# Kernel tuning notes

Hardware: AMD Instinct MI355X
Metric: run time of the kernel (lower is better)

Reference implementation:

```python
import jax, jax.numpy as jnp
import numpy as np

PI2 = 2.0 * np.pi
ZITTER = 1e-4
TEMP = 0.1          # tempering0
LIKERR_BOUND = (0.1, 1.0)
GUMBEL_EPS = 1e-20


def setup_inputs() -> dict:
    key = jax.random.key(0)
    ks = jax.random.split(key, 12)
    nb, nd, ndim, nch = 8, 768, 1, 3
    nmix, h, ns = 5, 10, 10
    def xavier(k, shape):
        fan_in, fan_out = shape[1], shape[0]
        lim = np.sqrt(6.0 / (fan_in + fan_out))
        return jax.random.uniform(k, shape, jnp.float32, -lim, lim)
    return {
        "xc": jax.random.normal(ks[0], (nb, nd, ndim, nch), jnp.float32),
        "yc": jax.random.normal(ks[1], (nb, nd, nch), jnp.float32),
        "mu": jax.random.uniform(ks[2], (nmix, ndim), jnp.float32),
        "inv_std": jax.random.uniform(ks[3], (nmix, ndim), jnp.float32),
        "likerr": jax.random.uniform(ks[4], (nch,), jnp.float32),
        "unif": jax.random.uniform(ks[5], (nb, ns, nch, nmix), jnp.float32),
        "W1": xavier(ks[6], (h, nmix + 1)), "b1": jnp.zeros((h,), jnp.float32),
        "W2": xavier(ks[7], (h, h * nch)), "b2": jnp.zeros((h,), jnp.float32),
        "W3": xavier(ks[8], (h, h)), "b3": jnp.zeros((h,), jnp.float32),
        "W4": xavier(ks[9], (h, h)), "b4": jnp.zeros((h,), jnp.float32),
        "W5": xavier(ks[10], (nmix * nch, h)), "b5": jnp.zeros((nmix * nch,), jnp.float32),
    }


def _sm_kernel_mix(xc, mu, inv_std):
    """Spectral-mixture kernel per mixture: (nb,nmix,nd,nd,nch)."""
    exp_x = xc[:, None] * inv_std[None, :, None, :, None]   # (nb,nmix,nd,ndim,nch)
    cos_x = xc[:, None] * mu[None, :, None, :, None]
    e2 = jnp.sum(exp_x ** 2, axis=-2)                        # (nb,nmix,nd,nch)
    cross = jnp.einsum('bmadk,bmcdk->bmack', exp_x, exp_x)   # (nb,nmix,nd,nd,nch)
    exp_term = e2[:, :, :, None, :] + e2[:, :, None, :, :] - 2.0 * cross
    c1 = jnp.sum(cos_x, axis=-2)                             # (nb,nmix,nd,nch)
    cos_term = c1[:, :, :, None, :] - c1[:, :, None, :, :]
    return jnp.exp(-0.5 * PI2 ** 2 * exp_term) * jnp.cos(PI2 * cos_term)


def reference(xc, yc, mu, inv_std, likerr, unif,
              W1, b1, W2, b2, W3, b3, W4, b4, W5, b5):
    nb, nd, ndim, nch = xc.shape
    nmix = mu.shape[0]
    outs = _sm_kernel_mix(xc, mu, inv_std)                   # (nb,nmix,nd,nd,nch)

    # --- trans-invariant weight net (logits=None kernel path + zitter eye) ---
    # feature[b,i,c,m] = sum_j (K + zitter*I)[b,m,i,j,c] * yc[b,j,c]
    feature = jnp.einsum('bmijc,bjc->bicm', outs, yc) + ZITTER * yc[:, :, :, None]
    tif = jnp.concatenate([feature, yc[..., None]], axis=-1) # (nb,nd,nch,nmix+1)
    hh = jax.nn.relu(tif @ W1.T + b1)                        # (nb,nd,nch,h)
    hh = hh.mean(axis=1).reshape(nb, -1)                     # (nb,nch*h)
    hh = jax.nn.relu(hh @ W2.T + b2)
    hh = jax.nn.relu(hh @ W3.T + b3)
    hh = jax.nn.relu(hh @ W4.T + b4)
    loglogits = (hh @ W5.T + b5).reshape(nb, nch, nmix)      # (nb,nch,nmix)

    # --- Gumbel-softmax mixture sampling ---
    g = -jnp.log(-jnp.log(unif + GUMBEL_EPS))                # (nb,ns,nch,nmix)
    y = jax.nn.softmax((g + loglogits[:, None]) / TEMP, axis=-1)
    logits_s = y.mean(axis=1)                                # (nb,nch,nmix)

    # --- weighted mixture reduction + noise diagonal ---
    w = jnp.transpose(logits_s, (0, 2, 1))[:, :, None, None, :]  # (nb,nmix,1,1,nch)
    weighted = jnp.sum(outs * w, axis=1)                     # (nb,nd,nd,nch)
    likerr_c = jnp.clip(likerr, LIKERR_BOUND[0], LIKERR_BOUND[1])
    eye = jnp.eye(nd, dtype=xc.dtype)
    weighted = weighted + (ZITTER + likerr_c ** 2)[None, None, None, :] * eye[None, :, :, None]
    return weighted
```

## Files before the change

kernel.cpp:

```cpp
#include <hip/hip_runtime.h>
#include <hip/hip_bf16.h>

#define NB 8
#define ND 768
#define NCH 3
#define NMIX 5
#define NH 10
#define NS 10

#define PI2F 6.283185307179586f
#define HALF_PI2SQ 19.739208802178716f
#define ZITTERF 1e-4f

__device__ __forceinline__ float cos2pi(float t) {
    return __builtin_amdgcn_cosf(__builtin_amdgcn_fractf(t));
}

__global__ void __launch_bounds__(256) feature_kernel(
        const float* __restrict__ xc, const float* __restrict__ yc,
        const float* __restrict__ mu, const float* __restrict__ istd,
        float* __restrict__ tif) {
    const int wid  = (blockIdx.x << 2) + (threadIdx.x >> 6);
    const int lane = threadIdx.x & 63;
    const int b   = wid / (ND * NCH);
    const int rem = wid % (ND * NCH);
    const int i = rem / NCH;
    const int c = rem % NCH;

    float cmu[NMIX], cexp[NMIX];
#pragma unroll
    for (int m = 0; m < NMIX; ++m) {
        const float is = istd[m];
        cmu[m]  = mu[m];
        cexp[m] = -HALF_PI2SQ * is * is;
    }

    const float xi = xc[(b * ND + i) * NCH + c];
    float acc[NMIX] = {0.f, 0.f, 0.f, 0.f, 0.f};

    for (int j = lane; j < ND; j += 64) {
        const float xj = xc[(b * ND + j) * NCH + c];
        const float yj = yc[(b * ND + j) * NCH + c];
        const float dx  = xi - xj;
        const float dx2 = dx * dx;
#pragma unroll
        for (int m = 0; m < NMIX; ++m) {
            const float e  = __expf(cexp[m] * dx2);
            const float co = cos2pi(cmu[m] * dx);
            acc[m] += e * co * yj;
        }
    }

#pragma unroll
    for (int m = 0; m < NMIX; ++m)
        for (int off = 32; off; off >>= 1)
            acc[m] += __shfl_down(acc[m], off);

    if (lane == 0) {
        const float yi = yc[(b * ND + i) * NCH + c];
        float* tp = tif + ((b * ND + i) * NCH + c) * (NMIX + 1);
#pragma unroll
        for (int m = 0; m < NMIX; ++m) tp[m] = acc[m] + ZITTERF * yi;
        tp[NMIX] = yi;
    }
}

__global__ void __launch_bounds__(256) mlp_gumbel_kernel(
        const float* __restrict__ tif,
        const float* __restrict__ W1, const float* __restrict__ b1,
        const float* __restrict__ W2, const float* __restrict__ b2,
        const float* __restrict__ W3, const float* __restrict__ b3,
        const float* __restrict__ W4, const float* __restrict__ b4,
        const float* __restrict__ W5, const float* __restrict__ b5,
        const float* __restrict__ unif,
        float* __restrict__ wout) {
    const int b   = blockIdx.x;
    const int tid = threadIdx.x;

    __shared__ float sW1[NH * 6], sb1[NH];
    __shared__ float red[4][NCH * NH];
    __shared__ float hvec[NCH * NH], h2[NH], h3[NH], h4[NH], ll[NCH * NMIX], wacc[NCH * NMIX];

    if (tid < NH * 6) sW1[tid] = W1[tid];
    if (tid < NH)     sb1[tid] = b1[tid];
    if (tid < NCH * NMIX) wacc[tid] = 0.f;
    __syncthreads();

    float part[NCH * NH];
#pragma unroll
    for (int t = 0; t < NCH * NH; ++t) part[t] = 0.f;

    for (int ii = tid; ii < ND; ii += 256) {
        for (int c = 0; c < NCH; ++c) {
            const float* tp = tif + ((b * ND + ii) * NCH + c) * (NMIX + 1);
            float f[6];
#pragma unroll
            for (int m = 0; m < 6; ++m) f[m] = tp[m];
#pragma unroll
            for (int k = 0; k < NH; ++k) {
                float a = sb1[k];
#pragma unroll
                for (int m = 0; m < 6; ++m) a += f[m] * sW1[k * 6 + m];
                part[c * NH + k] += fmaxf(a, 0.f);
            }
        }
    }

#pragma unroll
    for (int t = 0; t < NCH * NH; ++t)
        for (int off = 32; off; off >>= 1)
            part[t] += __shfl_down(part[t], off);

    const int lane = tid & 63, wv = tid >> 6;
    if (lane == 0)
        for (int t = 0; t < NCH * NH; ++t) red[wv][t] = part[t];
    __syncthreads();

    if (tid < NCH * NH)
        hvec[tid] = (red[0][tid] + red[1][tid] + red[2][tid] + red[3][tid]) * (1.f / (float)ND);
    __syncthreads();

    if (tid < NH) {
        float a = b2[tid];
        for (int j = 0; j < NCH * NH; ++j) a += W2[tid * (NCH * NH) + j] * hvec[j];
        h2[tid] = fmaxf(a, 0.f);
    }
    __syncthreads();
    if (tid < NH) {
        float a = b3[tid];
        for (int j = 0; j < NH; ++j) a += W3[tid * NH + j] * h2[j];
        h3[tid] = fmaxf(a, 0.f);
    }
    __syncthreads();
    if (tid < NH) {
        float a = b4[tid];
        for (int j = 0; j < NH; ++j) a += W4[tid * NH + j] * h3[j];
        h4[tid] = fmaxf(a, 0.f);
    }
    __syncthreads();
    if (tid < NCH * NMIX) {
        float a = b5[tid];
        for (int j = 0; j < NH; ++j) a += W5[tid * NH + j] * h4[j];
        ll[tid] = a;
    }
    __syncthreads();

    if (tid < NS * NCH) {
        const int s = tid / NCH, c = tid % NCH;
        float z[NMIX], zmax = -1e30f;
#pragma unroll
        for (int m = 0; m < NMIX; ++m) {
            const float u = unif[((b * NS + s) * NCH + c) * NMIX + m];
            const float g = -__logf(-__logf(u + 1e-20f));
            z[m] = (g + ll[c * NMIX + m]) * 10.0f;
            zmax = fmaxf(zmax, z[m]);
        }
        float e[NMIX], se = 0.f;
#pragma unroll
        for (int m = 0; m < NMIX; ++m) { e[m] = __expf(z[m] - zmax); se += e[m]; }
        const float inv = 0.1f / se;
#pragma unroll
        for (int m = 0; m < NMIX; ++m)
            atomicAdd(&wacc[c * NMIX + m], e[m] * inv);
    }
    __syncthreads();
    if (tid < NCH * NMIX) wout[b * (NCH * NMIX) + tid] = wacc[tid];
}

__global__ void __launch_bounds__(256) weighted_kernel(
        const float* __restrict__ xc, const float* __restrict__ wmix,
        const float* __restrict__ mu, const float* __restrict__ istd,
        const float* __restrict__ likerr,
        float* __restrict__ out) {
    const int b   = blockIdx.x / ((ND * ND) / 256);
    const int rem = blockIdx.x % ((ND * ND) / 256);
    const int i   = rem / (ND / 256);
    const int j   = (rem % (ND / 256)) * 256 + threadIdx.x;
    const int tid = threadIdx.x;

    __shared__ float sw[NCH * NMIX], smu[NMIX], sce[NMIX], sdiag[NCH], sxi[NCH];
    if (tid < NCH * NMIX) sw[tid] = wmix[b * (NCH * NMIX) + tid];
    if (tid < NMIX) {
        smu[tid] = mu[tid];
        const float is = istd[tid];
        sce[tid] = -HALF_PI2SQ * is * is;
    }
    if (tid < NCH) {
        const float lk = fminf(fmaxf(likerr[tid], 0.1f), 1.0f);
        sdiag[tid] = ZITTERF + lk * lk;
        sxi[tid]   = xc[(b * ND + i) * NCH + tid];
    }
    __syncthreads();

    float xj[NCH];
#pragma unroll
    for (int c = 0; c < NCH; ++c) xj[c] = xc[(b * ND + j) * NCH + c];

    float res[NCH];
#pragma unroll
    for (int c = 0; c < NCH; ++c) {
        const float dx  = sxi[c] - xj[c];
        const float dx2 = dx * dx;
        float a = 0.f;
#pragma unroll
        for (int m = 0; m < NMIX; ++m)
            a += sw[c * NMIX + m] * __expf(sce[m] * dx2) * cos2pi(smu[m] * dx);
        if (i == j) a += sdiag[c];
        res[c] = a;
    }

    float* op = out + (size_t)((b * ND + i) * ND + j) * NCH;
    op[0] = res[0];
    op[1] = res[1];
    op[2] = res[2];
}

extern "C" void kernel_launch(void* const* d_in, const int* in_sizes, int n_in,
                              void* d_out, int out_size, void* d_ws, size_t ws_size,
                              hipStream_t stream) {
    const float* xc     = (const float*)d_in[0];
    const float* yc     = (const float*)d_in[1];
    const float* mu     = (const float*)d_in[2];
    const float* istd   = (const float*)d_in[3];
    const float* likerr = (const float*)d_in[4];
    const float* unif   = (const float*)d_in[5];
    const float* W1 = (const float*)d_in[6];  const float* b1 = (const float*)d_in[7];
    const float* W2 = (const float*)d_in[8];  const float* b2 = (const float*)d_in[9];
    const float* W3 = (const float*)d_in[10]; const float* b3 = (const float*)d_in[11];
    const float* W4 = (const float*)d_in[12]; const float* b4 = (const float*)d_in[13];
    const float* W5 = (const float*)d_in[14]; const float* b5 = (const float*)d_in[15];

    float* out  = (float*)d_out;
    float* tif  = (float*)d_ws;
    float* wmix = tif + NB * ND * NCH * (NMIX + 1);

    feature_kernel<<<(NB * ND * NCH) / 4, 256, 0, stream>>>(xc, yc, mu, istd, tif);

    mlp_gumbel_kernel<<<NB, 256, 0, stream>>>(tif, W1, b1, W2, b2, W3, b3, W4, b4,
                                              W5, b5, unif, wmix);

    weighted_kernel<<<(NB * ND * ND) / 256, 256, 0, stream>>>(xc, wmix, mu, istd,
                                                              likerr, out);
}
```

Baseline: 150.0 us.

## Factor cosine differences via sin/cos products and tile four rows per wave/block

The cosine of a difference is expanded as cos(a)cos(b)+sin(a)sin(b), so per-point sin/cos values are computed once and reused across four rows in both the feature and output kernels, replacing one trig call per pair with two FMAs. Exponentials switch to native exp2 with a prescaled constant. The MLP weights are staged into shared memory with unrolled loops. The output kernel now does four rows per thread, which cuts the block count but raises register pressure. The trig factorization may also change numerical precision slightly.

```diff
diff --git a/kernel.cpp b/kernel.cpp
--- a/kernel.cpp
+++ b/kernel.cpp
@@ -8,12 +8,14 @@
 #define NH 10
 #define NS 10
 
-#define PI2F 6.283185307179586f
 #define HALF_PI2SQ 19.739208802178716f
+#define EXP2_SCALE 28.47780760903922f
 #define ZITTERF 1e-4f
 
-__device__ __forceinline__ float cos2pi(float t) {
-    return __builtin_amdgcn_cosf(__builtin_amdgcn_fractf(t));
+__device__ __forceinline__ void sincos2pi(float t, float& s, float& c) {
+    const float f = __builtin_amdgcn_fractf(t);
+    s = __builtin_amdgcn_sinf(f);
+    c = __builtin_amdgcn_cosf(f);
 }
 
 __global__ void __launch_bounds__(256) feature_kernel(
@@ -22,46 +24,70 @@
         float* __restrict__ tif) {
     const int wid  = (blockIdx.x << 2) + (threadIdx.x >> 6);
     const int lane = threadIdx.x & 63;
-    const int b   = wid / (ND * NCH);
-    const int rem = wid % (ND * NCH);
-    const int i = rem / NCH;
-    const int c = rem % NCH;
-
-    float cmu[NMIX], cexp[NMIX];
+    const int b   = wid / (NCH * (ND / 4));
+    const int rem = wid % (NCH * (ND / 4));
+    const int c   = rem / (ND / 4);
+    const int i0  = (rem % (ND / 4)) * 4;
+
+    float cmu[NMIX], ce2[NMIX];
 #pragma unroll
     for (int m = 0; m < NMIX; ++m) {
         const float is = istd[m];
-        cmu[m]  = mu[m];
-        cexp[m] = -HALF_PI2SQ * is * is;
-    }
-
-    const float xi = xc[(b * ND + i) * NCH + c];
-    float acc[NMIX] = {0.f, 0.f, 0.f, 0.f, 0.f};
+        cmu[m] = mu[m];
+        ce2[m] = -EXP2_SCALE * is * is;
+    }
+
+    float xi[4], ci[4][NMIX], si[4][NMIX];
+#pragma unroll
+    for (int t = 0; t < 4; ++t) {
+        xi[t] = xc[(b * ND + i0 + t) * NCH + c];
+#pragma unroll
+        for (int m = 0; m < NMIX; ++m)
+            sincos2pi(cmu[m] * xi[t], si[t][m], ci[t][m]);
+    }
+
+    float acc[4][NMIX];
+#pragma unroll
+    for (int t = 0; t < 4; ++t)
+#pragma unroll
+        for (int m = 0; m < NMIX; ++m) acc[t][m] = 0.f;
 
     for (int j = lane; j < ND; j += 64) {
         const float xj = xc[(b * ND + j) * NCH + c];
         const float yj = yc[(b * ND + j) * NCH + c];
-        const float dx  = xi - xj;
-        const float dx2 = dx * dx;
-#pragma unroll
-        for (int m = 0; m < NMIX; ++m) {
-            const float e  = __expf(cexp[m] * dx2);
-            const float co = cos2pi(cmu[m] * dx);
-            acc[m] += e * co * yj;
-        }
-    }
-
-#pragma unroll
-    for (int m = 0; m < NMIX; ++m)
-        for (int off = 32; off; off >>= 1)
-            acc[m] += __shfl_down(acc[m], off);
+        float cj[NMIX], sj[NMIX];
+#pragma unroll
+        for (int m = 0; m < NMIX; ++m)
+            sincos2pi(cmu[m] * xj, sj[m], cj[m]);
+#pragma unroll
+        for (int t = 0; t < 4; ++t) {
+            const float dx  = xi[t] - xj;
+            const float dx2 = dx * dx;
+#pragma unroll
+            for (int m = 0; m < NMIX; ++m) {
+                const float e  = __builtin_amdgcn_exp2f(ce2[m] * dx2);
+                const float cv = fmaf(ci[t][m], cj[m], si[t][m] * sj[m]);
+                acc[t][m] = fmaf(e * cv, yj, acc[t][m]);
+            }
+        }
+    }
+
+#pragma unroll
+    for (int t = 0; t < 4; ++t)
+#pragma unroll
+        for (int m = 0; m < NMIX; ++m)
+            for (int off = 32; off; off >>= 1)
+                acc[t][m] += __shfl_down(acc[t][m], off);
 
     if (lane == 0) {
-        const float yi = yc[(b * ND + i) * NCH + c];
-        float* tp = tif + ((b * ND + i) * NCH + c) * (NMIX + 1);
-#pragma unroll
-        for (int m = 0; m < NMIX; ++m) tp[m] = acc[m] + ZITTERF * yi;
-        tp[NMIX] = yi;
+#pragma unroll
+        for (int t = 0; t < 4; ++t) {
+            const float yi = yc[(b * ND + i0 + t) * NCH + c];
+            float* tp = tif + ((b * ND + i0 + t) * NCH + c) * (NMIX + 1);
+#pragma unroll
+            for (int m = 0; m < NMIX; ++m) tp[m] = acc[t][m] + ZITTERF * yi;
+            tp[NMIX] = yi;
+        }
     }
 }
 
@@ -77,13 +103,19 @@
     const int b   = blockIdx.x;
     const int tid = threadIdx.x;
 
-    __shared__ float sW1[NH * 6], sb1[NH];
+    __shared__ float sW1[NH * 6], sW2[NH * NCH * NH], sW3[NH * NH], sW4[NH * NH],
+                     sW5[NCH * NMIX * NH];
+    __shared__ float sb1[NH], sb2[NH], sb3[NH], sb4[NH], sb5[NCH * NMIX];
     __shared__ float red[4][NCH * NH];
     __shared__ float hvec[NCH * NH], h2[NH], h3[NH], h4[NH], ll[NCH * NMIX], wacc[NCH * NMIX];
 
     if (tid < NH * 6) sW1[tid] = W1[tid];
-    if (tid < NH)     sb1[tid] = b1[tid];
-    if (tid < NCH * NMIX) wacc[tid] = 0.f;
+    for (int t = tid; t < NH * NCH * NH; t += 256) sW2[t] = W2[t];
+    if (tid < NH * NH) sW3[tid] = W3[tid];
+    if (tid < NH * NH) sW4[tid] = W4[tid];
+    if (tid < NCH * NMIX * NH) sW5[tid] = W5[tid];
+    if (tid < NH) { sb1[tid] = b1[tid]; sb2[tid] = b2[tid]; sb3[tid] = b3[tid]; sb4[tid] = b4[tid]; }
+    if (tid < NCH * NMIX) { sb5[tid] = b5[tid]; wacc[tid] = 0.f; }
     __syncthreads();
 
     float part[NCH * NH];
@@ -121,26 +153,30 @@
     __syncthreads();
 
     if (tid < NH) {
-        float a = b2[tid];
-        for (int j = 0; j < NCH * NH; ++j) a += W2[tid * (NCH * NH) + j] * hvec[j];
+        float a = sb2[tid];
+#pragma unroll
+        for (int j = 0; j < NCH * NH; ++j) a += sW2[tid * (NCH * NH) + j] * hvec[j];
         h2[tid] = fmaxf(a, 0.f);
     }
     __syncthreads();
     if (tid < NH) {
-        float a = b3[tid];
-        for (int j = 0; j < NH; ++j) a += W3[tid * NH + j] * h2[j];
+        float a = sb3[tid];
+#pragma unroll
+        for (int j = 0; j < NH; ++j) a += sW3[tid * NH + j] * h2[j];
         h3[tid] = fmaxf(a, 0.f);
     }
     __syncthreads();
     if (tid < NH) {
-        float a = b4[tid];
-        for (int j = 0; j < NH; ++j) a += W4[tid * NH + j] * h3[j];
+        float a = sb4[tid];
+#pragma unroll
+        for (int j = 0; j < NH; ++j) a += sW4[tid * NH + j] * h3[j];
         h4[tid] = fmaxf(a, 0.f);
     }
     __syncthreads();
     if (tid < NCH * NMIX) {
-        float a = b5[tid];
-        for (int j = 0; j < NH; ++j) a += W5[tid * NH + j] * h4[j];
+        float a = sb5[tid];
+#pragma unroll
+        for (int j = 0; j < NH; ++j) a += sW5[tid * NH + j] * h4[j];
         ll[tid] = a;
     }
     __syncthreads();
@@ -172,47 +208,74 @@
         const float* __restrict__ mu, const float* __restrict__ istd,
         const float* __restrict__ likerr,
         float* __restrict__ out) {
-    const int b   = blockIdx.x / ((ND * ND) / 256);
-    const int rem = blockIdx.x % ((ND * ND) / 256);
-    const int i   = rem / (ND / 256);
+    const int b   = blockIdx.x / ((ND / 4) * (ND / 256));
+    const int rem = blockIdx.x % ((ND / 4) * (ND / 256));
+    const int i0  = (rem / (ND / 256)) * 4;
     const int j   = (rem % (ND / 256)) * 256 + threadIdx.x;
     const int tid = threadIdx.x;
 
-    __shared__ float sw[NCH * NMIX], smu[NMIX], sce[NMIX], sdiag[NCH], sxi[NCH];
-    if (tid < NCH * NMIX) sw[tid] = wmix[b * (NCH * NMIX) + tid];
-    if (tid < NMIX) {
-        smu[tid] = mu[tid];
-        const float is = istd[tid];
-        sce[tid] = -HALF_PI2SQ * is * is;
-    }
-    if (tid < NCH) {
-        const float lk = fminf(fmaxf(likerr[tid], 0.1f), 1.0f);
-        sdiag[tid] = ZITTERF + lk * lk;
-        sxi[tid]   = xc[(b * ND + i) * NCH + tid];
-    }
-    __syncthreads();
-
-    float xj[NCH];
-#pragma unroll
-    for (int c = 0; c < NCH; ++c) xj[c] = xc[(b * ND + j) * NCH + c];
-
-    float res[NCH];
+    __shared__ float2 strig[4][NCH][NMIX];
+
+    if (tid < 4 * NCH * NMIX) {
+        const int it = tid / (NCH * NMIX);
+        const int r  = tid % (NCH * NMIX);
+        const int cc = r / NMIX, m = r % NMIX;
+        const float x = xc[(b * ND + i0 + it) * NCH + cc];
+        float s, co;
+        sincos2pi(mu[m] * x, s, co);
+        strig[it][cc][m] = make_float2(co, s);
+    }
+    __syncthreads();
+
+    float cmu[NMIX], ce2[NMIX], w[NCH * NMIX], diag[NCH];
+#pragma unroll
+    for (int m = 0; m < NMIX; ++m) {
+        const float is = istd[m];
+        cmu[m] = mu[m];
+        ce2[m] = -EXP2_SCALE * is * is;
+    }
+#pragma unroll
+    for (int t = 0; t < NCH * NMIX; ++t) w[t] = wmix[b * (NCH * NMIX) + t];
 #pragma unroll
     for (int c = 0; c < NCH; ++c) {
-        const float dx  = sxi[c] - xj[c];
-        const float dx2 = dx * dx;
-        float a = 0.f;
-#pragma unroll
-        for (int m = 0; m < NMIX; ++m)
-            a += sw[c * NMIX + m] * __expf(sce[m] * dx2) * cos2pi(smu[m] * dx);
-        if (i == j) a += sdiag[c];
-        res[c] = a;
-    }
-
-    float* op = out + (size_t)((b * ND + i) * ND + j) * NCH;
-    op[0] = res[0];
-    op[1] = res[1];
-    op[2] = res[2];
+        const float lk = fminf(fmaxf(likerr[c], 0.1f), 1.0f);
+        diag[c] = ZITTERF + lk * lk;
+    }
+
+    float xj[NCH], cj[NCH][NMIX], sj[NCH][NMIX];
+#pragma unroll
+    for (int c = 0; c < NCH; ++c) {
+        xj[c] = xc[(b * ND + j) * NCH + c];
+#pragma unroll
+        for (int m = 0; m < NMIX; ++m)
+            sincos2pi(cmu[m] * xj[c], sj[c][m], cj[c][m]);
+    }
+
+#pragma unroll
+    for (int it = 0; it < 4; ++it) {
+        const int i = i0 + it;
+        float res[NCH];
+#pragma unroll
+        for (int c = 0; c < NCH; ++c) {
+            const float xi  = xc[(b * ND + i) * NCH + c];
+            const float dx  = xi - xj[c];
+            const float dx2 = dx * dx;
+            float a = 0.f;
+#pragma unroll
+            for (int m = 0; m < NMIX; ++m) {
+                const float2 t2 = strig[it][c][m];
+                const float e   = __builtin_amdgcn_exp2f(ce2[m] * dx2);
+                const float cv  = fmaf(t2.x, cj[c][m], t2.y * sj[c][m]);
+                a = fmaf(w[c * NMIX + m], e * cv, a);
+            }
+            if (i == j) a += diag[c];
+            res[c] = a;
+        }
+        float* op = out + (size_t)((b * ND + i) * ND + j) * NCH;
+        op[0] = res[0];
+        op[1] = res[1];
+        op[2] = res[2];
+    }
 }
 
 extern "C" void kernel_launch(void* const* d_in, const int* in_sizes, int n_in,
@@ -234,11 +297,11 @@
     float* tif  = (float*)d_ws;
     float* wmix = tif + NB * ND * NCH * (NMIX + 1);
 
-    feature_kernel<<<(NB * ND * NCH) / 4, 256, 0, stream>>>(xc, yc, mu, istd, tif);
+    feature_kernel<<<(NB * NCH * (ND / 4)) / 4, 256, 0, stream>>>(xc, yc, mu, istd, tif);
 
     mlp_gumbel_kernel<<<NB, 256, 0, stream>>>(tif, W1, b1, W2, b2, W3, b3, W4, b4,
                                               W5, b5, unif, wmix);
 
-    weighted_kernel<<<(NB * ND * ND) / 256, 256, 0, stream>>>(xc, wmix, mu, istd,
-                                                              likerr, out);
-}
+    weighted_kernel<<<NB * (ND / 4) * (ND / 256), 256, 0, stream>>>(xc, wmix, mu, istd,
+                                                                    likerr, out);
+}
```

After: 150.6 us. Within noise of the previous version (+0.4%).
